# Kernel tuning notes

Measured on AMD Instinct MI355X. Metric: run time of the kernel, lower is better.

The kernel has to match this reference:

```python
import jax, jax.numpy as jnp
import numpy as np

B, VD, SD, CD, H, HEADS = 16384, 2048, 1024, 512, 256, 4
DH = H // HEADS
EPS = 1e-5


def layer_norm(x, g, b):
    m = jnp.mean(x, axis=-1, keepdims=True)
    v = jnp.var(x, axis=-1, keepdims=True)
    return (x - m) * jax.lax.rsqrt(v + EPS) * g + b


def setup_inputs() -> dict:
    key = jax.random.key(0)
    ks = jax.random.split(key, 16)
    sc = 0.02
    inp = {
        'fv': jax.random.normal(ks[0], (B, VD), jnp.float32),
        'fs': jax.random.normal(ks[1], (B, SD), jnp.float32),
        'fc': jax.random.normal(ks[2], (B, CD), jnp.float32),
        # projection linears + layernorms
        'Wv': jax.random.normal(ks[3], (H, VD), jnp.float32) * sc,
        'bv': jnp.zeros((H,), jnp.float32),
        'gv': jnp.ones((H,), jnp.float32), 'bev': jnp.zeros((H,), jnp.float32),
        'Ws': jax.random.normal(ks[4], (H, SD), jnp.float32) * sc,
        'bs': jnp.zeros((H,), jnp.float32),
        'gs': jnp.ones((H,), jnp.float32), 'bes': jnp.zeros((H,), jnp.float32),
        'Wc': jax.random.normal(ks[5], (H, CD), jnp.float32) * sc,
        'bc': jnp.zeros((H,), jnp.float32),
        'gc_': jnp.ones((H,), jnp.float32), 'bec': jnp.zeros((H,), jnp.float32),
        # MultiheadAttention packed in-proj and out-proj
        'in_w': jax.random.normal(ks[6], (3 * H, H), jnp.float32) * sc,
        'in_b': jnp.zeros((3 * H,), jnp.float32),
        'out_w': jax.random.normal(ks[7], (H, H), jnp.float32) * sc,
        'out_b': jnp.zeros((H,), jnp.float32),
        # post-attention layernorm
        'gn': jnp.ones((H,), jnp.float32), 'gb': jnp.zeros((H,), jnp.float32),
        # gating MLP: Linear(3H,64) -> GELU -> Linear(64,3) -> softmax
        'g1w': jax.random.normal(ks[8], (64, 3 * H), jnp.float32) * sc,
        'g1b': jnp.zeros((64,), jnp.float32),
        'g2w': jax.random.normal(ks[9], (3, 64), jnp.float32) * sc,
        'g2b': jnp.zeros((3,), jnp.float32),
    }
    return inp


def reference(fv, fs, fc, Wv, bv, gv, bev, Ws, bs, gs, bes, Wc, bc, gc_, bec,
              in_w, in_b, out_w, out_b, gn, gb, g1w, g1b, g2w, g2b):
    v = layer_norm(fv @ Wv.T + bv, gv, bev)   # [B,H]
    s = layer_norm(fs @ Ws.T + bs, gs, bes)
    c = layer_norm(fc @ Wc.T + bc, gc_, bec)
    stack = jnp.stack([v, s, c], axis=1)      # [B,3,H]

    # self-attention over seq=3 (eval mode: dropout off)
    qkv = stack @ in_w.T + in_b               # [B,3,3H]
    q, k, vv = jnp.split(qkv, 3, axis=-1)
    def heads(x):  # [B,3,H] -> [B,HEADS,3,DH]
        return x.reshape(B, 3, HEADS, DH).transpose(0, 2, 1, 3)
    q, k, vv = heads(q), heads(k), heads(vv)
    scores = jnp.einsum('bhqd,bhkd->bhqk', q, k) / jnp.sqrt(jnp.float32(DH))
    attn = jax.nn.softmax(scores, axis=-1)
    ctx = jnp.einsum('bhqk,bhkd->bhqd', attn, vv)
    ctx = ctx.transpose(0, 2, 1, 3).reshape(B, 3, H)
    attended = ctx @ out_w.T + out_b          # [B,3,H]

    attended = layer_norm(attended + stack, gn, gb)
    av, as_, ac = attended[:, 0], attended[:, 1], attended[:, 2]

    h1 = jax.nn.gelu(jnp.concatenate([av, as_, ac], axis=-1) @ g1w.T + g1b, approximate=False)
    gates = jax.nn.softmax(h1 @ g2w.T + g2b, axis=-1)  # [B,3]

    fused = gates[:, 0:1] * av + gates[:, 1:2] * as_ + gates[:, 2:3] * ac
    return (fused, gates)
```

## Files before the change

kernel.cpp:

```cpp
#include <hip/hip_runtime.h>
#include <math.h>


typedef unsigned short u16;
typedef __bf16 bf16x8 __attribute__((ext_vector_type(8)));
typedef float fx4 __attribute__((ext_vector_type(4)));

#define MFMA_BF16(A_, B_, C_) __builtin_amdgcn_mfma_f32_16x16x32_bf16((A_), (B_), (C_), 0, 0, 0)

__device__ __forceinline__ float bf2f(u16 s) {
    union { float f; unsigned u; } c; c.u = ((unsigned)s) << 16; return c.f;
}
__device__ __forceinline__ u16 f2bf(float f) {
    union { float f; unsigned u; } c; c.f = f;
    return (u16)((c.u + 0x7fffu + ((c.u >> 16) & 1u)) >> 16);
}
__device__ __forceinline__ float bfpair_dot(unsigned a, unsigned b) {
    union { unsigned u; float f; } al, ah, bl, bh;
    al.u = a << 16; ah.u = a & 0xffff0000u;
    bl.u = b << 16; bh.u = b & 0xffff0000u;
    return al.f * bl.f + ah.f * bh.f;
}
__device__ __forceinline__ void gld16(void* l, const void* g) {
    __builtin_amdgcn_global_load_lds((const __attribute__((address_space(1))) void*)g,
                                     (__attribute__((address_space(3))) void*)l, 16, 0, 0);
}

__global__ __launch_bounds__(256) void cvt_w(const float* Wv, const float* Ws, const float* Wc,
                                             const float* inw, const float* outw, const float* g1w,
                                             u16* dst) {
    int idx = blockIdx.x * 256 + threadIdx.x;
    const float* src; int rel;
    if      (idx <  524288) { src = Wv;   rel = idx; }
    else if (idx <  786432) { src = Ws;   rel = idx -  524288; }
    else if (idx <  917504) { src = Wc;   rel = idx -  786432; }
    else if (idx < 1114112) { src = inw;  rel = idx -  917504; }
    else if (idx < 1179648) { src = outw; rel = idx - 1114112; }
    else                    { src = g1w;  rel = idx - 1179648; }
    dst[idx] = f2bf(src[rel]);
}

__global__ __launch_bounds__(256, 3) void gemm_ln(
    const float* fv, const float* fs, const float* fc,
    const u16* wWv, const u16* wWs, const u16* wWc,
    const float* bv, const float* gv, const float* bev,
    const float* bs, const float* gs, const float* bes,
    const float* bc, const float* gc_, const float* bec,
    u16* stack) {
    __shared__ alignas(16) char smem[45568];
    u16* sC = (u16*)smem;
    float* redS = (float*)(smem + 43008);
    float* redQ = (float*)(smem + 44032);
    float* mvS  = (float*)(smem + 45056);

    int bid = blockIdx.x;
    int slot, mblk;
    if (bid < 256)      { slot = 0; mblk = bid; }
    else if (bid < 512) { slot = 1; mblk = bid - 256; }
    else                { slot = 2; mblk = bid - 512; }

    const float* A; const u16* W; const float* bias; const float* gg; const float* be; int K;
    if (slot == 0)      { A = fv; W = wWv; bias = bv; gg = gv;  be = bev; K = 2048; }
    else if (slot == 1) { A = fs; W = wWs; bias = bs; gg = gs;  be = bes; K = 1024; }
    else                { A = fc; W = wWc; bias = bc; gg = gc_; be = bec; K = 512;  }

    int t = threadIdx.x, wv = t >> 6, ln = t & 63, q = ln >> 4, l15 = ln & 15;
    int m0 = mblk * 64;

    fx4 zero = {0.f, 0.f, 0.f, 0.f};
    fx4 acc[4][4];
    #pragma unroll
    for (int mi = 0; mi < 4; ++mi)
        #pragma unroll
        for (int ni = 0; ni < 4; ++ni) acc[mi][ni] = zero;

    int rowA = t >> 2, ca = t & 3;
    const float* aBase = A + (size_t)(m0 + rowA) * K + ca * 8;
    int sAwOff = rowA * 40 + ca * 8;

    int bN[4], bKc[4], bDst[4];
    #pragma unroll
    for (int i = 0; i < 4; ++i) {
        int d = wv * 256 + i * 64 + ln;
        bN[i] = d >> 2;
        bKc[i] = (d & 3) ^ ((bN[i] >> 1) & 3);
        bDst[i] = (wv * 256 + i * 64) * 16;
    }

    int niter = K >> 5;

    {
        float4 f0 = *(const float4*)(aBase);
        float4 f1 = *(const float4*)(aBase + 4);
        #pragma unroll
        for (int i = 0; i < 4; ++i)
            gld16(smem + 10240 + bDst[i], W + (size_t)bN[i] * K + bKc[i] * 8);
        union { u16 us[8]; uint4 v; } pk;
        pk.us[0] = f2bf(f0.x); pk.us[1] = f2bf(f0.y); pk.us[2] = f2bf(f0.z); pk.us[3] = f2bf(f0.w);
        pk.us[4] = f2bf(f1.x); pk.us[5] = f2bf(f1.y); pk.us[6] = f2bf(f1.z); pk.us[7] = f2bf(f1.w);
        *(uint4*)((u16*)smem + sAwOff) = pk.v;
    }
    __syncthreads();

    for (int kt = 0; kt < niter; ++kt) {
        int cur = kt & 1, nxt_b = (kt + 1) & 1;
        u16* sAc = (u16*)(smem + cur * 5120);
        u16* sBc = (u16*)(smem + 10240 + cur * 16384);
        int has_next = (kt + 1) < niter;

        float4 nf0, nf1;
        if (has_next) {
            nf0 = *(const float4*)(aBase + (kt + 1) * 32);
            nf1 = *(const float4*)(aBase + (kt + 1) * 32 + 4);
            char* sBn = smem + 10240 + nxt_b * 16384;
            #pragma unroll
            for (int i = 0; i < 4; ++i)
                gld16(sBn + bDst[i], W + (size_t)bN[i] * K + (kt + 1) * 32 + bKc[i] * 8);
        }

        bf16x8 af[4], bfr[4];
        #pragma unroll
        for (int mi = 0; mi < 4; ++mi)
            af[mi] = *(const bf16x8*)(sAc + (mi * 16 + l15) * 40 + q * 8);
        #pragma unroll
        for (int ni = 0; ni < 4; ++ni) {
            int n = wv * 64 + ni * 16 + l15;
            int ch = n * 4 + (q ^ ((n >> 1) & 3));
            bfr[ni] = *(const bf16x8*)(sBc + ch * 8);
        }
        #pragma unroll
        for (int mi = 0; mi < 4; ++mi)
            #pragma unroll
            for (int ni = 0; ni < 4; ++ni)
                acc[mi][ni] = MFMA_BF16(af[mi], bfr[ni], acc[mi][ni]);

        if (has_next) {
            union { u16 us[8]; uint4 v; } pk;
            pk.us[0] = f2bf(nf0.x); pk.us[1] = f2bf(nf0.y); pk.us[2] = f2bf(nf0.z); pk.us[3] = f2bf(nf0.w);
            pk.us[4] = f2bf(nf1.x); pk.us[5] = f2bf(nf1.y); pk.us[6] = f2bf(nf1.z); pk.us[7] = f2bf(nf1.w);
            *(uint4*)((u16*)(smem + nxt_b * 5120) + sAwOff) = pk.v;
        }
        __syncthreads();
    }

    float biasv[4], gvv[4], bevv[4];
    #pragma unroll
    for (int ni = 0; ni < 4; ++ni) {
        int col = wv * 64 + ni * 16 + l15;
        biasv[ni] = bias[col]; gvv[ni] = gg[col]; bevv[ni] = be[col];
    }
    #pragma unroll
    for (int mi = 0; mi < 4; ++mi)
        #pragma unroll
        for (int ni = 0; ni < 4; ++ni)
            #pragma unroll
            for (int r = 0; r < 4; ++r) acc[mi][ni][r] += biasv[ni];
    #pragma unroll
    for (int mi = 0; mi < 4; ++mi) {
        #pragma unroll
        for (int r = 0; r < 4; ++r) {
            float s = 0.f, qq = 0.f;
            #pragma unroll
            for (int ni = 0; ni < 4; ++ni) { float x = acc[mi][ni][r]; s += x; qq += x * x; }
            #pragma unroll
            for (int m = 1; m < 16; m <<= 1) { s += __shfl_xor(s, m, 64); qq += __shfl_xor(qq, m, 64); }
            if (l15 == 0) { int rho = mi * 16 + q * 4 + r; redS[rho * 4 + wv] = s; redQ[rho * 4 + wv] = qq; }
        }
    }
    __syncthreads();
    if (t < 64) {
        float s = redS[t * 4] + redS[t * 4 + 1] + redS[t * 4 + 2] + redS[t * 4 + 3];
        float qq = redQ[t * 4] + redQ[t * 4 + 1] + redQ[t * 4 + 2] + redQ[t * 4 + 3];
        float mean = s * (1.f / 256.f);
        float var = qq * (1.f / 256.f) - mean * mean;
        mvS[t * 2] = mean; mvS[t * 2 + 1] = rsqrtf(var + 1e-5f);
    }
    __syncthreads();
    #pragma unroll
    for (int mi = 0; mi < 4; ++mi) {
        #pragma unroll
        for (int r = 0; r < 4; ++r) {
            int rho = mi * 16 + q * 4 + r;
            float mean = mvS[rho * 2], rstd = mvS[rho * 2 + 1];
            #pragma unroll
            for (int ni = 0; ni < 4; ++ni) {
                int col = wv * 64 + ni * 16 + l15;
                float x = (acc[mi][ni][r] - mean) * rstd * gvv[ni] + bevv[ni];
                sC[rho * 256 + col] = f2bf(x);
            }
        }
    }
    __syncthreads();
    u16* outp = stack + (size_t)m0 * 768 + slot * 256;
    #pragma unroll
    for (int it = 0; it < 8; ++it) {
        int idx = t + it * 256;
        int row = idx >> 5, c = idx & 31;
        uint4 v = *(const uint4*)(sC + row * 256 + c * 8);
        *(uint4*)(outp + (size_t)row * 768 + c * 8) = v;
    }
}

__global__ __launch_bounds__(256) void gemm_qkv(const u16* stack, const u16* W, const float* in_b,
                                                u16* qkv) {
    __shared__ alignas(16) char smem[32768];
    u16* sC = (u16*)smem;

    int t = threadIdx.x, wv = t >> 6, ln = t & 63, q = ln >> 4, l15 = ln & 15;
    int n0 = blockIdx.x * 128, m0 = blockIdx.y * 128;
    int wr = wv >> 1, wc = wv & 1;

    fx4 zero = {0.f, 0.f, 0.f, 0.f};
    fx4 acc[4][4];
    #pragma unroll
    for (int mi = 0; mi < 4; ++mi)
        #pragma unroll
        for (int ni = 0; ni < 4; ++ni) acc[mi][ni] = zero;

    int sR[2], sKc[2], sDst[2];
    #pragma unroll
    for (int i = 0; i < 2; ++i) {
        int d = wv * 128 + i * 64 + ln;
        sR[i] = d >> 2;
        sKc[i] = (d & 3) ^ ((sR[i] >> 1) & 3);
        sDst[i] = (wv * 128 + i * 64) * 16;
    }

    #pragma unroll
    for (int i = 0; i < 2; ++i) {
        gld16(smem + sDst[i],         stack + (size_t)(m0 + sR[i]) * 256 + sKc[i] * 8);
        gld16(smem + 16384 + sDst[i], W     + (size_t)(n0 + sR[i]) * 256 + sKc[i] * 8);
    }
    __syncthreads();

    for (int kt = 0; kt < 8; ++kt) {
        int cur = kt & 1, nxt_b = (kt + 1) & 1;
        if (kt < 7) {
            #pragma unroll
            for (int i = 0; i < 2; ++i) {
                gld16(smem + nxt_b * 8192 + sDst[i],
                      stack + (size_t)(m0 + sR[i]) * 256 + (kt + 1) * 32 + sKc[i] * 8);
                gld16(smem + 16384 + nxt_b * 8192 + sDst[i],
                      W + (size_t)(n0 + sR[i]) * 256 + (kt + 1) * 32 + sKc[i] * 8);
            }
        }
        u16* sAc = (u16*)(smem + cur * 8192);
        u16* sBc = (u16*)(smem + 16384 + cur * 8192);
        bf16x8 af[4], bfr[4];
        #pragma unroll
        for (int mi = 0; mi < 4; ++mi) {
            int r = wr * 64 + mi * 16 + l15;
            int ch = r * 4 + (q ^ ((r >> 1) & 3));
            af[mi] = *(const bf16x8*)(sAc + ch * 8);
        }
        #pragma unroll
        for (int ni = 0; ni < 4; ++ni) {
            int n = wc * 64 + ni * 16 + l15;
            int ch = n * 4 + (q ^ ((n >> 1) & 3));
            bfr[ni] = *(const bf16x8*)(sBc + ch * 8);
        }
        #pragma unroll
        for (int mi = 0; mi < 4; ++mi)
            #pragma unroll
            for (int ni = 0; ni < 4; ++ni)
                acc[mi][ni] = MFMA_BF16(af[mi], bfr[ni], acc[mi][ni]);
        __syncthreads();
    }
    float biasv[4];
    #pragma unroll
    for (int ni = 0; ni < 4; ++ni) biasv[ni] = in_b[n0 + wc * 64 + ni * 16 + l15];
    #pragma unroll
    for (int mi = 0; mi < 4; ++mi)
        #pragma unroll
        for (int ni = 0; ni < 4; ++ni)
            #pragma unroll
            for (int r = 0; r < 4; ++r) {
                int rl = wr * 64 + mi * 16 + q * 4 + r;
                int cl = wc * 64 + ni * 16 + l15;
                sC[rl * 128 + cl] = f2bf(acc[mi][ni][r] + biasv[ni]);
            }
    __syncthreads();
    #pragma unroll
    for (int it = 0; it < 8; ++it) {
        int idx = t + it * 256;
        int row = idx >> 4, c = idx & 15;
        uint4 v = *(const uint4*)(sC + row * 128 + c * 8);
        *(uint4*)(qkv + (size_t)(m0 + row) * 768 + n0 + c * 8) = v;
    }
}

__global__ __launch_bounds__(256) void attn_k(const u16* qkv, u16* ctx) {
    __shared__ alignas(16) char smem[38016];
    u16* qs = (u16*)smem;
    float* sS = (float*)(smem + 36864);

    int t = threadIdx.x, wv = t >> 6, ln = t & 63;
    size_t base = (size_t)blockIdx.x * 8 * 2304;
    #pragma unroll
    for (int i = 0; i < 9; ++i) {
        int d = wv * 576 + i * 64;
        gld16((char*)smem + (size_t)d * 16, qkv + base + (size_t)(d + ln) * 8);
    }
    __syncthreads();
    #pragma unroll
    for (int it = 0; it < 2; ++it) {
        int idx = t + it * 256;
        if (idx < 288) {
            int b = idx / 36, rem = idx % 36, h = rem / 9, pp = rem % 9, i = pp / 3, j = pp % 3;
            const u16* qp = qs + b * 2304 + i * 768 + h * 64;
            const u16* kp = qs + b * 2304 + j * 768 + 256 + h * 64;
            float acc = 0.f;
            #pragma unroll
            for (int c = 0; c < 8; ++c) {
                uint4 qa = *(const uint4*)(qp + c * 8);
                uint4 ka = *(const uint4*)(kp + c * 8);
                acc += bfpair_dot(qa.x, ka.x) + bfpair_dot(qa.y, ka.y) +
                       bfpair_dot(qa.z, ka.z) + bfpair_dot(qa.w, ka.w);
            }
            sS[idx] = acc * 0.125f;
        }
    }
    __syncthreads();
    if (t < 96) {
        int b3 = t * 3;
        float s0 = sS[b3], s1 = sS[b3 + 1], s2 = sS[b3 + 2];
        float m = fmaxf(s0, fmaxf(s1, s2));
        float e0 = __expf(s0 - m), e1 = __expf(s1 - m), e2 = __expf(s2 - m);
        float inv = 1.f / (e0 + e1 + e2);
        sS[b3] = e0 * inv; sS[b3 + 1] = e1 * inv; sS[b3 + 2] = e2 * inv;
    }
    __syncthreads();
    #pragma unroll
    for (int it = 0; it < 3; ++it) {
        int idx = t + it * 256;
        int b = idx / 96, rem = idx % 96, i = rem / 32, c = rem & 31, h = c >> 3;
        int pbase = b * 36 + h * 9 + i * 3;
        float o[8];
        #pragma unroll
        for (int e = 0; e < 8; ++e) o[e] = 0.f;
        #pragma unroll
        for (int j = 0; j < 3; ++j) {
            float p = sS[pbase + j];
            uint4 va = *(const uint4*)(qs + b * 2304 + j * 768 + 512 + c * 8);
            unsigned uu[4] = {va.x, va.y, va.z, va.w};
            #pragma unroll
            for (int pr = 0; pr < 4; ++pr) {
                union { unsigned u; float f; } lo, hi;
                lo.u = uu[pr] << 16; hi.u = uu[pr] & 0xffff0000u;
                o[2 * pr]     += p * lo.f;
                o[2 * pr + 1] += p * hi.f;
            }
        }
        union { u16 us[8]; uint4 v; } pk;
        #pragma unroll
        for (int e = 0; e < 8; ++e) pk.us[e] = f2bf(o[e]);
        *(uint4*)(ctx + (size_t)(blockIdx.x * 8 + b) * 768 + i * 256 + c * 8) = pk.v;
    }
}

__global__ __launch_bounds__(256) void outproj_k(
    const u16* ctx, const u16* W, const float* out_b, const u16* stack,
    const float* gn, const float* gb, const u16* g1w, const float* g1b,
    const float* g2w, const float* g2b, float* outF, float* outG) {
    __shared__ alignas(16) char smem[40960];
    u16* r1 = (u16*)smem;
    u16* sB = (u16*)(smem + 24576);
    float* redS = (float*)(smem + 24576);
    float* redQ = redS + 192;
    float* mvS = redQ + 192;
    float* h1S = (float*)(smem + 26624);
    float* lgS = (float*)(smem + 30720);
    float* gateS = lgS + 48;

    int t = threadIdx.x, wv = t >> 6, ln = t & 63, q = ln >> 4, l15 = ln & 15;
    int gr0 = blockIdx.x * 48, b0 = blockIdx.x * 16;

    #pragma unroll
    for (int i = 0; i < 6; ++i) {
        int d = wv * 384 + i * 64 + ln;
        int row = d >> 5, p = d & 31;
        int kc = p ^ (row & 7);
        gld16((char*)r1 + (wv * 384 + i * 64) * 16, ctx + (size_t)(gr0 + row) * 256 + kc * 8);
    }
    __syncthreads();

    fx4 zero = {0.f, 0.f, 0.f, 0.f};
    fx4 acc[3][4];
    #pragma unroll
    for (int mi = 0; mi < 3; ++mi)
        #pragma unroll
        for (int ni = 0; ni < 4; ++ni) acc[mi][ni] = zero;

    for (int kt = 0; kt < 8; ++kt) {
        #pragma unroll
        for (int i = 0; i < 4; ++i) {
            int d = wv * 256 + i * 64 + ln;
            int n = d >> 2, p = d & 3;
            int kc = p ^ ((n >> 1) & 3);
            gld16((char*)sB + (wv * 256 + i * 64) * 16, W + (size_t)n * 256 + kt * 32 + kc * 8);
        }
        __syncthreads();
        bf16x8 af[3], bfr[4];
        #pragma unroll
        for (int mi = 0; mi < 3; ++mi) {
            int row = mi * 16 + l15;
            int ch = row * 32 + ((kt * 4 + q) ^ (row & 7));
            af[mi] = *(const bf16x8*)(r1 + ch * 8);
        }
        #pragma unroll
        for (int ni = 0; ni < 4; ++ni) {
            int n = wv * 64 + ni * 16 + l15;
            int ch = n * 4 + (q ^ ((n >> 1) & 3));
            bfr[ni] = *(const bf16x8*)(sB + ch * 8);
        }
        #pragma unroll
        for (int mi = 0; mi < 3; ++mi)
            #pragma unroll
            for (int ni = 0; ni < 4; ++ni)
                acc[mi][ni] = MFMA_BF16(af[mi], bfr[ni], acc[mi][ni]);
        __syncthreads();
    }

    #pragma unroll
    for (int i = 0; i < 6; ++i) {
        int d = wv * 384 + i * 64 + ln;
        gld16((char*)r1 + (wv * 384 + i * 64) * 16, stack + (size_t)gr0 * 256 + (size_t)d * 8);
    }
    __syncthreads();

    float obv[4], gnv[4], gbv[4];
    #pragma unroll
    for (int ni = 0; ni < 4; ++ni) {
        int col = wv * 64 + ni * 16 + l15;
        obv[ni] = out_b[col]; gnv[ni] = gn[col]; gbv[ni] = gb[col];
    }
    #pragma unroll
    for (int mi = 0; mi < 3; ++mi)
        #pragma unroll
        for (int ni = 0; ni < 4; ++ni)
            #pragma unroll
            for (int r = 0; r < 4; ++r) {
                int rho = mi * 16 + q * 4 + r;
                int col = wv * 64 + ni * 16 + l15;
                acc[mi][ni][r] += obv[ni] + bf2f(r1[rho * 256 + col]);
            }
    #pragma unroll
    for (int mi = 0; mi < 3; ++mi) {
        #pragma unroll
        for (int r = 0; r < 4; ++r) {
            float s = 0.f, qq = 0.f;
            #pragma unroll
            for (int ni = 0; ni < 4; ++ni) { float x = acc[mi][ni][r]; s += x; qq += x * x; }
            #pragma unroll
            for (int m = 1; m < 16; m <<= 1) { s += __shfl_xor(s, m, 64); qq += __shfl_xor(qq, m, 64); }
            if (l15 == 0) { int rho = mi * 16 + q * 4 + r; redS[rho * 4 + wv] = s; redQ[rho * 4 + wv] = qq; }
        }
    }
    __syncthreads();
    if (t < 48) {
        float s = redS[t * 4] + redS[t * 4 + 1] + redS[t * 4 + 2] + redS[t * 4 + 3];
        float qq = redQ[t * 4] + redQ[t * 4 + 1] + redQ[t * 4 + 2] + redQ[t * 4 + 3];
        float mean = s * (1.f / 256.f);
        float var = qq * (1.f / 256.f) - mean * mean;
        mvS[t * 2] = mean; mvS[t * 2 + 1] = rsqrtf(var + 1e-5f);
    }
    __syncthreads();
    #pragma unroll
    for (int mi = 0; mi < 3; ++mi) {
        #pragma unroll
        for (int r = 0; r < 4; ++r) {
            int rho = mi * 16 + q * 4 + r;
            float mean = mvS[rho * 2], rstd = mvS[rho * 2 + 1];
            int bl = rho / 3, sl = rho - bl * 3;
            #pragma unroll
            for (int ni = 0; ni < 4; ++ni) {
                int col = wv * 64 + ni * 16 + l15;
                float x = (acc[mi][ni][r] - mean) * rstd * gnv[ni] + gbv[ni];
                int k = sl * 256 + col;
                int kidx = k >> 3, wn = k & 7;
                r1[(bl * 96 + (kidx ^ (bl & 7))) * 8 + wn] = f2bf(x);
            }
        }
    }
    __syncthreads();
    fx4 ag = zero;
    for (int kt = 0; kt < 24; ++kt) {
        int bl = l15;
        int kidx = kt * 4 + q;
        bf16x8 afr = *(const bf16x8*)(r1 + (bl * 96 + (kidx ^ (bl & 7))) * 8);
        int n = wv * 16 + l15;
        bf16x8 bfr2 = *(const bf16x8*)(g1w + (size_t)n * 768 + kt * 32 + q * 8);
        ag = MFMA_BF16(afr, bfr2, ag);
    }
    #pragma unroll
    for (int r = 0; r < 4; ++r) {
        int bl = q * 4 + r, n = wv * 16 + l15;
        float x = ag[r] + g1b[n];
        h1S[bl * 64 + n] = 0.5f * x * (1.f + erff(x * 0.70710678118f));
    }
    __syncthreads();
    if (t < 48) {
        int bl = t / 3, s = t - bl * 3;
        float a = g2b[s];
        #pragma unroll
        for (int k = 0; k < 64; ++k) a += h1S[bl * 64 + k] * g2w[s * 64 + k];
        lgS[t] = a;
    }
    __syncthreads();
    if (t < 48) {
        int bl = t / 3, s = t - bl * 3;
        float l0 = lgS[bl * 3], l1 = lgS[bl * 3 + 1], l2 = lgS[bl * 3 + 2];
        float m = fmaxf(l0, fmaxf(l1, l2));
        float e0 = __expf(l0 - m), e1 = __expf(l1 - m), e2 = __expf(l2 - m);
        float inv = 1.f / (e0 + e1 + e2);
        float gsel = ((s == 0) ? e0 : (s == 1) ? e1 : e2) * inv;
        gateS[t] = gsel;
        outG[(size_t)(b0 + bl) * 3 + s] = gsel;
    }
    __syncthreads();
    #pragma unroll
    for (int it = 0; it < 2; ++it) {
        int idx = t + it * 256;
        int b = idx >> 5, c = idx & 31;
        float g0 = gateS[b * 3], g1 = gateS[b * 3 + 1], g2 = gateS[b * 3 + 2];
        float o[8];
        #pragma unroll
        for (int e = 0; e < 8; ++e) o[e] = 0.f;
        #pragma unroll
        for (int s = 0; s < 3; ++s) {
            float gw = (s == 0) ? g0 : (s == 1) ? g1 : g2;
            int kidx = s * 32 + c;
            uint4 raw = *(const uint4*)(r1 + (b * 96 + (kidx ^ (b & 7))) * 8);
            unsigned uu[4] = {raw.x, raw.y, raw.z, raw.w};
            #pragma unroll
            for (int pr = 0; pr < 4; ++pr) {
                union { unsigned u; float f; } lo, hi;
                lo.u = uu[pr] << 16; hi.u = uu[pr] & 0xffff0000u;
                o[2 * pr]     += gw * lo.f;
                o[2 * pr + 1] += gw * hi.f;
            }
        }
        float* op = outF + (size_t)(b0 + b) * 256 + c * 8;
        float4 v0; v0.x = o[0]; v0.y = o[1]; v0.z = o[2]; v0.w = o[3];
        float4 v1; v1.x = o[4]; v1.y = o[5]; v1.z = o[6]; v1.w = o[7];
        *(float4*)op = v0;
        *(float4*)(op + 4) = v1;
    }
}

extern "C" void kernel_launch(void* const* d_in, const int* in_sizes, int n_in,
                              void* d_out, int out_size, void* d_ws, size_t ws_size,
                              hipStream_t stream) {
    (void)in_sizes; (void)n_in; (void)out_size; (void)ws_size;
    const float* fv   = (const float*)d_in[0];
    const float* fs   = (const float*)d_in[1];
    const float* fc   = (const float*)d_in[2];
    const float* Wv   = (const float*)d_in[3];
    const float* bv   = (const float*)d_in[4];
    const float* gv   = (const float*)d_in[5];
    const float* bev  = (const float*)d_in[6];
    const float* Ws   = (const float*)d_in[7];
    const float* bs   = (const float*)d_in[8];
    const float* gs   = (const float*)d_in[9];
    const float* bes  = (const float*)d_in[10];
    const float* Wc   = (const float*)d_in[11];
    const float* bc   = (const float*)d_in[12];
    const float* gc_  = (const float*)d_in[13];
    const float* bec  = (const float*)d_in[14];
    const float* in_w = (const float*)d_in[15];
    const float* in_b = (const float*)d_in[16];
    const float* out_w= (const float*)d_in[17];
    const float* out_b= (const float*)d_in[18];
    const float* gn   = (const float*)d_in[19];
    const float* gb   = (const float*)d_in[20];
    const float* g1w  = (const float*)d_in[21];
    const float* g1b  = (const float*)d_in[22];
    const float* g2w  = (const float*)d_in[23];
    const float* g2b  = (const float*)d_in[24];

    u16* w0    = (u16*)d_ws;
    u16* wWv   = w0;
    u16* wWs   = w0 + 524288;
    u16* wWc   = w0 + 786432;
    u16* wIn   = w0 + 917504;
    u16* wOut  = w0 + 1114112;
    u16* wG1   = w0 + 1179648;
    u16* stack = w0 + 1228800;
    u16* qkv   = w0 + 13811712;
    u16* ctx   = w0 + 51560448;
    float* outF = (float*)d_out;
    float* outG = outF + (size_t)16384 * 256;

    cvt_w<<<4800, 256, 0, stream>>>(Wv, Ws, Wc, in_w, out_w, g1w, w0);
    gemm_ln<<<768, 256, 0, stream>>>(fv, fs, fc, wWv, wWs, wWc,
                                     bv, gv, bev, bs, gs, bes, bc, gc_, bec, stack);
    gemm_qkv<<<dim3(6, 384), 256, 0, stream>>>(stack, wIn, in_b, qkv);
    attn_k<<<2048, 256, 0, stream>>>(qkv, ctx);
    outproj_k<<<1024, 256, 0, stream>>>(ctx, wOut, out_b, stack, gn, gb,
                                        wG1, g1b, g2w, g2b, outF, outG);
}
```

Baseline: 438.1 us.

## Fuse attention into out-projection kernel and triple-buffer QKV GEMM loads

Removes the separate attention kernel: the out-projection kernel now loads Q/K for 16 batch rows, computes scores and softmax, then loads V into the same LDS region and writes the context directly into the swizzled LDS tile used by the out-proj GEMM. This drops the ctx round trip through global memory and one launch. Separately, the QKV GEMM moves from double to triple buffering with explicit vmcnt waits, one barrier per k-step, and raised MFMA priority. In exchange both kernels use more LDS (64KB and 48KB), which may lower occupancy.

```diff
diff --git a/kernel.cpp b/kernel.cpp
--- a/kernel.cpp
+++ b/kernel.cpp
@@ -7,6 +7,7 @@
 typedef float fx4 __attribute__((ext_vector_type(4)));
 
 #define MFMA_BF16(A_, B_, C_) __builtin_amdgcn_mfma_f32_16x16x32_bf16((A_), (B_), (C_), 0, 0, 0)
+#define WAIT_VM(N) asm volatile("s_waitcnt vmcnt(" #N ")" ::: "memory")
 
 __device__ __forceinline__ float bf2f(u16 s) {
     union { float f; unsigned u; } c; c.u = ((unsigned)s) << 16; return c.f;
@@ -201,9 +202,9 @@
     }
 }
 
-__global__ __launch_bounds__(256) void gemm_qkv(const u16* stack, const u16* W, const float* in_b,
-                                                u16* qkv) {
-    __shared__ alignas(16) char smem[32768];
+__global__ __launch_bounds__(256, 3) void gemm_qkv(const u16* stack, const u16* W, const float* in_b,
+                                                   u16* qkv) {
+    __shared__ alignas(16) char smem[49152];
     u16* sC = (u16*)smem;
 
     int t = threadIdx.x, wv = t >> 6, ln = t & 63, q = ln >> 4, l15 = ln & 15;
@@ -217,35 +218,40 @@
         #pragma unroll
         for (int ni = 0; ni < 4; ++ni) acc[mi][ni] = zero;
 
-    int sR[2], sKc[2], sDst[2];
+    int sR[2], sKc[2];
     #pragma unroll
     for (int i = 0; i < 2; ++i) {
         int d = wv * 128 + i * 64 + ln;
         sR[i] = d >> 2;
         sKc[i] = (d & 3) ^ ((sR[i] >> 1) & 3);
-        sDst[i] = (wv * 128 + i * 64) * 16;
-    }
-
-    #pragma unroll
-    for (int i = 0; i < 2; ++i) {
-        gld16(smem + sDst[i],         stack + (size_t)(m0 + sR[i]) * 256 + sKc[i] * 8);
-        gld16(smem + 16384 + sDst[i], W     + (size_t)(n0 + sR[i]) * 256 + sKc[i] * 8);
-    }
-    __syncthreads();
-
+    }
+
+#define QK_ISSUE(ktile, bufoff)                                                         \
+    {                                                                                   \
+        char* bA_ = smem + (bufoff);                                                    \
+        char* bB_ = bA_ + 8192;                                                         \
+        _Pragma("unroll")                                                               \
+        for (int i_ = 0; i_ < 2; ++i_) {                                                \
+            gld16(bA_ + (wv * 128 + i_ * 64) * 16,                                      \
+                  stack + (size_t)(m0 + sR[i_]) * 256 + (ktile) * 32 + sKc[i_] * 8);    \
+            gld16(bB_ + (wv * 128 + i_ * 64) * 16,                                      \
+                  W + (size_t)(n0 + sR[i_]) * 256 + (ktile) * 32 + sKc[i_] * 8);        \
+        }                                                                               \
+    }
+
+    QK_ISSUE(0, 0);
+    QK_ISSUE(1, 16384);
+    int cb = 0;
     for (int kt = 0; kt < 8; ++kt) {
-        int cur = kt & 1, nxt_b = (kt + 1) & 1;
-        if (kt < 7) {
-            #pragma unroll
-            for (int i = 0; i < 2; ++i) {
-                gld16(smem + nxt_b * 8192 + sDst[i],
-                      stack + (size_t)(m0 + sR[i]) * 256 + (kt + 1) * 32 + sKc[i] * 8);
-                gld16(smem + 16384 + nxt_b * 8192 + sDst[i],
-                      W + (size_t)(n0 + sR[i]) * 256 + (kt + 1) * 32 + sKc[i] * 8);
-            }
-        }
-        u16* sAc = (u16*)(smem + cur * 8192);
-        u16* sBc = (u16*)(smem + 16384 + cur * 8192);
+        if (kt < 7) { WAIT_VM(4); } else { WAIT_VM(0); }
+        __builtin_amdgcn_sched_barrier(0);
+        __builtin_amdgcn_s_barrier();
+        __builtin_amdgcn_sched_barrier(0);
+        int nb = cb + 2; if (nb >= 3) nb -= 3;
+        if (kt + 2 < 8) QK_ISSUE(kt + 2, nb * 16384);
+
+        const u16* sAc = (const u16*)(smem + cb * 16384);
+        const u16* sBc = (const u16*)(smem + cb * 16384 + 8192);
         bf16x8 af[4], bfr[4];
         #pragma unroll
         for (int mi = 0; mi < 4; ++mi) {
@@ -259,13 +265,18 @@
             int ch = n * 4 + (q ^ ((n >> 1) & 3));
             bfr[ni] = *(const bf16x8*)(sBc + ch * 8);
         }
+        __builtin_amdgcn_s_setprio(1);
         #pragma unroll
         for (int mi = 0; mi < 4; ++mi)
             #pragma unroll
             for (int ni = 0; ni < 4; ++ni)
                 acc[mi][ni] = MFMA_BF16(af[mi], bfr[ni], acc[mi][ni]);
-        __syncthreads();
-    }
+        __builtin_amdgcn_s_setprio(0);
+        cb += 1; if (cb >= 3) cb -= 3;
+    }
+#undef QK_ISSUE
+    __syncthreads();
+
     float biasv[4];
     #pragma unroll
     for (int ni = 0; ni < 4; ++ni) biasv[ni] = in_b[n0 + wc * 64 + ni * 16 + l15];
@@ -289,26 +300,40 @@
     }
 }
 
-__global__ __launch_bounds__(256) void attn_k(const u16* qkv, u16* ctx) {
-    __shared__ alignas(16) char smem[38016];
-    u16* qs = (u16*)smem;
-    float* sS = (float*)(smem + 36864);
-
-    int t = threadIdx.x, wv = t >> 6, ln = t & 63;
-    size_t base = (size_t)blockIdx.x * 8 * 2304;
-    #pragma unroll
-    for (int i = 0; i < 9; ++i) {
-        int d = wv * 576 + i * 64;
-        gld16((char*)smem + (size_t)d * 16, qkv + base + (size_t)(d + ln) * 8);
-    }
-    __syncthreads();
-    #pragma unroll
-    for (int it = 0; it < 2; ++it) {
+__global__ __launch_bounds__(256) void outproj_k(
+    const u16* qkv, const u16* W, const float* out_b, const u16* stack,
+    const float* gn, const float* gb, const u16* g1w, const float* g1b,
+    const float* g2w, const float* g2b, float* outF, float* outG) {
+    __shared__ alignas(16) char smem[65536];
+    u16* qk  = (u16*)smem;
+    u16* vb  = (u16*)smem;
+    u16* r1  = (u16*)(smem + 24576);
+    u16* sB  = (u16*)(smem + 49152);
+    float* sS   = (float*)(smem + 49152);
+    float* redS = (float*)(smem + 49152);
+    float* redQ = (float*)(smem + 49920);
+    float* mvS  = (float*)(smem + 50688);
+    float* h1S  = (float*)(smem + 51072);
+    float* lgS  = (float*)(smem + 55168);
+    float* gateS= (float*)(smem + 55360);
+
+    int t = threadIdx.x, wv = t >> 6, ln = t & 63, q = ln >> 4, l15 = ln & 15;
+    int gr0 = blockIdx.x * 48, b0 = blockIdx.x * 16;
+
+    #pragma unroll
+    for (int i = 0; i < 12; ++i) {
+        int d = i * 256 + t;
+        int row = d >> 6, cc = d & 63;
+        gld16((char*)smem + d * 16, qkv + (size_t)(gr0 + row) * 768 + cc * 8);
+    }
+    __syncthreads();
+    #pragma unroll
+    for (int it = 0; it < 3; ++it) {
         int idx = t + it * 256;
-        if (idx < 288) {
+        if (idx < 576) {
             int b = idx / 36, rem = idx % 36, h = rem / 9, pp = rem % 9, i = pp / 3, j = pp % 3;
-            const u16* qp = qs + b * 2304 + i * 768 + h * 64;
-            const u16* kp = qs + b * 2304 + j * 768 + 256 + h * 64;
+            const u16* qp = qk + (b * 3 + i) * 512 + h * 64;
+            const u16* kp = qk + (b * 3 + j) * 512 + 256 + h * 64;
             float acc = 0.f;
             #pragma unroll
             for (int c = 0; c < 8; ++c) {
@@ -321,7 +346,13 @@
         }
     }
     __syncthreads();
-    if (t < 96) {
+    #pragma unroll
+    for (int i = 0; i < 6; ++i) {
+        int d = i * 256 + t;
+        int row = d >> 5, cc = d & 31;
+        gld16((char*)smem + d * 16, qkv + (size_t)(gr0 + row) * 768 + 512 + cc * 8);
+    }
+    if (t < 192) {
         int b3 = t * 3;
         float s0 = sS[b3], s1 = sS[b3 + 1], s2 = sS[b3 + 2];
         float m = fmaxf(s0, fmaxf(s1, s2));
@@ -331,7 +362,7 @@
     }
     __syncthreads();
     #pragma unroll
-    for (int it = 0; it < 3; ++it) {
+    for (int it = 0; it < 6; ++it) {
         int idx = t + it * 256;
         int b = idx / 96, rem = idx % 96, i = rem / 32, c = rem & 31, h = c >> 3;
         int pbase = b * 36 + h * 9 + i * 3;
@@ -341,7 +372,7 @@
         #pragma unroll
         for (int j = 0; j < 3; ++j) {
             float p = sS[pbase + j];
-            uint4 va = *(const uint4*)(qs + b * 2304 + j * 768 + 512 + c * 8);
+            uint4 va = *(const uint4*)(vb + (b * 3 + j) * 256 + c * 8);
             unsigned uu[4] = {va.x, va.y, va.z, va.w};
             #pragma unroll
             for (int pr = 0; pr < 4; ++pr) {
@@ -354,33 +385,8 @@
         union { u16 us[8]; uint4 v; } pk;
         #pragma unroll
         for (int e = 0; e < 8; ++e) pk.us[e] = f2bf(o[e]);
-        *(uint4*)(ctx + (size_t)(blockIdx.x * 8 + b) * 768 + i * 256 + c * 8) = pk.v;
-    }
-}
-
-__global__ __launch_bounds__(256) void outproj_k(
-    const u16* ctx, const u16* W, const float* out_b, const u16* stack,
-    const float* gn, const float* gb, const u16* g1w, const float* g1b,
-    const float* g2w, const float* g2b, float* outF, float* outG) {
-    __shared__ alignas(16) char smem[40960];
-    u16* r1 = (u16*)smem;
-    u16* sB = (u16*)(smem + 24576);
-    float* redS = (float*)(smem + 24576);
-    float* redQ = redS + 192;
-    float* mvS = redQ + 192;
-    float* h1S = (float*)(smem + 26624);
-    float* lgS = (float*)(smem + 30720);
-    float* gateS = lgS + 48;
-
-    int t = threadIdx.x, wv = t >> 6, ln = t & 63, q = ln >> 4, l15 = ln & 15;
-    int gr0 = blockIdx.x * 48, b0 = blockIdx.x * 16;
-
-    #pragma unroll
-    for (int i = 0; i < 6; ++i) {
-        int d = wv * 384 + i * 64 + ln;
-        int row = d >> 5, p = d & 31;
-        int kc = p ^ (row & 7);
-        gld16((char*)r1 + (wv * 384 + i * 64) * 16, ctx + (size_t)(gr0 + row) * 256 + kc * 8);
+        int row = b * 3 + i;
+        *(uint4*)(r1 + (row * 32 + (c ^ (row & 7))) * 8) = pk.v;
     }
     __syncthreads();
 
@@ -587,7 +593,6 @@
     u16* wG1   = w0 + 1179648;
     u16* stack = w0 + 1228800;
     u16* qkv   = w0 + 13811712;
-    u16* ctx   = w0 + 51560448;
     float* outF = (float*)d_out;
     float* outG = outF + (size_t)16384 * 256;
 
@@ -595,7 +600,6 @@
     gemm_ln<<<768, 256, 0, stream>>>(fv, fs, fc, wWv, wWs, wWc,
                                      bv, gv, bev, bs, gs, bes, bc, gc_, bec, stack);
     gemm_qkv<<<dim3(6, 384), 256, 0, stream>>>(stack, wIn, in_b, qkv);
-    attn_k<<<2048, 256, 0, stream>>>(qkv, ctx);
-    outproj_k<<<1024, 256, 0, stream>>>(ctx, wOut, out_b, stack, gn, gb,
+    outproj_k<<<1024, 256, 0, stream>>>(qkv, wOut, out_b, stack, gn, gb,
                                         wG1, g1b, g2w, g2b, outF, outG);
 }
```

Result: faster. 421.2 us (-3.9%).
